# Kernel tuning notes

Hardware: AMD Instinct MI355X
Metric: run time of the kernel (lower is better)

The kernel has to match this reference:

```python
import jax, jax.numpy as jnp
import numpy as np

NQ, NKV, D = 32, 8, 64
HID = 2048
EPS = 1e-5
THETA = 1000000.0


def _rmsnorm(x, w):
    var = jnp.mean(x * x, axis=-1, keepdims=True)
    return x * jax.lax.rsqrt(var + EPS) * w


def setup_inputs() -> dict:
    key = jax.random.key(0)
    k1, k2, k3 = jax.random.split(key, 3)
    T = 2048
    positions = jnp.arange(T, dtype=jnp.int64) if jax.config.jax_enable_x64 else jnp.arange(T, dtype=jnp.int32)
    hidden_states = jax.random.normal(k1, (T, HID), dtype=jnp.float32)
    w_qkv = jax.random.normal(k2, (HID, (NQ + 2 * NKV) * D), dtype=jnp.float32) / np.sqrt(HID)
    w_out = jax.random.normal(k3, (NQ * D, HID), dtype=jnp.float32) / np.sqrt(NQ * D)
    q_ln_w = jnp.ones((D,), dtype=jnp.float32)
    k_ln_w = jnp.ones((D,), dtype=jnp.float32)
    return {"positions": positions, "hidden_states": hidden_states, "w_qkv": w_qkv,
            "w_out": w_out, "q_ln_w": q_ln_w, "k_ln_w": k_ln_w}


def reference(positions, hidden_states, w_qkv, w_out, q_ln_w, k_ln_w):
    T = hidden_states.shape[0]
    qkv = hidden_states @ w_qkv  # [T, (NQ+2*NKV)*D]
    q = qkv[:, : NQ * D].reshape(T, NQ, D)
    k = qkv[:, NQ * D : (NQ + NKV) * D].reshape(T, NKV, D)
    v = qkv[:, (NQ + NKV) * D :].reshape(T, NKV, D)
    # per-head RMSNorm on q and k
    q = _rmsnorm(q, q_ln_w)
    k = _rmsnorm(k, k_ln_w)
    # neox-style RoPE (rotate halves)
    inv_freq = 1.0 / (THETA ** (jnp.arange(0, D, 2, dtype=jnp.float32) / D))
    ang = positions.astype(jnp.float32)[:, None] * inv_freq  # [T, D/2]
    cos = jnp.cos(ang)[:, None, :]
    sin = jnp.sin(ang)[:, None, :]
    def rope(x):
        x1, x2 = x[..., : D // 2], x[..., D // 2 :]
        return jnp.concatenate([x1 * cos - x2 * sin, x2 * cos + x1 * sin], axis=-1)
    q = rope(q)
    k = rope(k)
    # grouped-query causal attention (one sequence, positions define order)
    G = NQ // NKV
    qg = q.reshape(T, NKV, G, D)
    scores = jnp.einsum('tkgd,skd->kgts', qg, k) * (D ** -0.5)  # [NKV,G,T,T]
    causal = jnp.arange(T)[:, None] >= jnp.arange(T)[None, :]
    scores = jnp.where(causal[None, None], scores, -1e30)
    probs = jax.nn.softmax(scores, axis=-1)
    attn = jnp.einsum('kgts,skd->tkgd', probs, v).reshape(T, NQ * D)
    return attn @ w_out
```

## Files before the change

### kernel.cpp

```cpp
#include <hip/hip_runtime.h>

typedef __bf16 bhalf;
typedef __bf16 bhalf8 __attribute__((ext_vector_type(8)));
typedef __bf16 bhalf4 __attribute__((ext_vector_type(4)));
typedef float f32x4 __attribute__((ext_vector_type(4)));

typedef __attribute__((address_space(1))) const void* gas_p;
typedef __attribute__((address_space(3))) void* las_p;

#define T_SEQ 2048
#define HIDN  2048
#define NQH   32
#define NKVH  8
#define DH    64
#define NQKV  3072

__global__ __launch_bounds__(256) void cast_bf16_k(const float* __restrict__ in,
                                                   bhalf* __restrict__ out, int n) {
  int i = (blockIdx.x * 256 + threadIdx.x) * 4;
  if (i + 3 < n) {
    float4 v = *(const float4*)(in + i);
    bhalf4 o;
    o[0] = (bhalf)v.x; o[1] = (bhalf)v.y; o[2] = (bhalf)v.z; o[3] = (bhalf)v.w;
    *(bhalf4*)(out + i) = o;
  }
}

__global__ __launch_bounds__(256) void transpose_cast_k(const float* __restrict__ in,
                                                        bhalf* __restrict__ out, int R, int C) {
  __shared__ float tile[32][33];
  int bx = blockIdx.x * 32;
  int by = blockIdx.y * 32;
  int tx = threadIdx.x & 31, ty = threadIdx.x >> 5;
#pragma unroll
  for (int p = 0; p < 4; ++p)
    tile[ty + 8 * p][tx] = in[(size_t)(by + ty + 8 * p) * C + bx + tx];
  __syncthreads();
#pragma unroll
  for (int p = 0; p < 4; ++p)
    out[(size_t)(bx + ty + 8 * p) * R + by + tx] = (bhalf)tile[tx][ty + 8 * p];
}

__global__ __launch_bounds__(256) void transpose_bf16_k(const bhalf* __restrict__ in,
                                                        bhalf* __restrict__ out, int R, int C) {
  __shared__ bhalf tile[32][33];
  int bx = blockIdx.x * 32;
  int by = blockIdx.y * 32;
  int tx = threadIdx.x & 31, ty = threadIdx.x >> 5;
#pragma unroll
  for (int p = 0; p < 4; ++p)
    tile[ty + 8 * p][tx] = in[(size_t)(by + ty + 8 * p) * C + bx + tx];
  __syncthreads();
#pragma unroll
  for (int p = 0; p < 4; ++p)
    out[(size_t)(bx + ty + 8 * p) * R + by + tx] = tile[tx][ty + 8 * p];
}

__device__ __forceinline__ void gemm_core(const bhalf* __restrict__ A,
                                          const bhalf* __restrict__ Bt, int K,
                                          int bm, int bn, int tid,
                                          bhalf* As, bhalf* Bs, f32x4 acc[2][4]) {
  int lane = tid & 63, wv = tid >> 6;
  int m16 = lane & 15, q4 = lane >> 4;
  int srow = tid >> 3;
  int scol = ((tid & 7) ^ (srow & 7)) * 8;
  const bhalf* asrc = A + (size_t)(bm + srow) * K + scol;
  const bhalf* bsrc = Bt + (size_t)(bn + srow) * K + scol;
  bhalf* adst = As + (wv * 8) * 64;
  bhalf* bdst = Bs + (wv * 8) * 64;
  int swz = m16 & 7;

  auto stage = [&](int k0, int sbuf) {
#pragma unroll
    for (int c = 0; c < 4; ++c)
      __builtin_amdgcn_global_load_lds((gas_p)(asrc + (size_t)(c * 32) * K + k0),
                                       (las_p)(adst + sbuf * 8192 + c * 2048), 16, 0, 0);
#pragma unroll
    for (int c = 0; c < 2; ++c)
      __builtin_amdgcn_global_load_lds((gas_p)(bsrc + (size_t)(c * 32) * K + k0),
                                       (las_p)(bdst + sbuf * 4096 + c * 2048), 16, 0, 0);
  };

  stage(0, 0);
  int buf = 0;
  for (int k0 = 0; k0 < K; k0 += 64) {
    __syncthreads();
    if (k0 + 64 < K) stage(k0 + 64, buf ^ 1);
    const bhalf* Ab = As + buf * 8192;
    const bhalf* Bb = Bs + buf * 4096;
    bhalf8 af[2][2], bf[4][2];
#pragma unroll
    for (int mi = 0; mi < 2; ++mi)
#pragma unroll
      for (int ks = 0; ks < 2; ++ks)
        af[mi][ks] = *(const bhalf8*)&Ab[(wv * 32 + mi * 16 + m16) * 64 +
                                         (((ks * 4 + q4) ^ swz) * 8)];
#pragma unroll
    for (int ni = 0; ni < 4; ++ni)
#pragma unroll
      for (int ks = 0; ks < 2; ++ks)
        bf[ni][ks] = *(const bhalf8*)&Bb[(ni * 16 + m16) * 64 +
                                         (((ks * 4 + q4) ^ swz) * 8)];
#pragma unroll
    for (int mi = 0; mi < 2; ++mi)
#pragma unroll
      for (int ni = 0; ni < 4; ++ni) {
        acc[mi][ni] = __builtin_amdgcn_mfma_f32_16x16x32_bf16(af[mi][0], bf[ni][0], acc[mi][ni], 0, 0, 0);
        acc[mi][ni] = __builtin_amdgcn_mfma_f32_16x16x32_bf16(af[mi][1], bf[ni][1], acc[mi][ni], 0, 0, 0);
      }
    buf ^= 1;
  }
}

__global__ __launch_bounds__(256) void gemm1_fused_k(const bhalf* __restrict__ A,
                                                     const bhalf* __restrict__ Bt,
                                                     const int* __restrict__ pos,
                                                     const float* __restrict__ qw,
                                                     const float* __restrict__ kw,
                                                     bhalf* __restrict__ qo,
                                                     bhalf* __restrict__ ko,
                                                     bhalf* __restrict__ vo) {
  __shared__ __align__(16) bhalf As[2 * 128 * 64];
  __shared__ __align__(16) bhalf Bs[2 * 64 * 64];
  int tid = threadIdx.x, lane = tid & 63, wv = tid >> 6;
  int m16 = lane & 15, q4 = lane >> 4;
  int bm = blockIdx.y * 128, bn = blockIdx.x * 64, h = blockIdx.x;
  f32x4 zero4 = {0.f, 0.f, 0.f, 0.f};
  f32x4 acc[2][4];
#pragma unroll
  for (int mi = 0; mi < 2; ++mi)
#pragma unroll
    for (int ni = 0; ni < 4; ++ni) acc[mi][ni] = zero4;

  gemm_core(A, Bt, HIDN, bm, bn, tid, As, Bs, acc);

  int wr0 = wv * 32;
  if (h < 40) {
    float wd[4];
    const float* wptr = (h < 32) ? qw : kw;
#pragma unroll
    for (int ni = 0; ni < 4; ++ni) wd[ni] = wptr[ni * 16 + m16];
    float f0 = exp2f((float)m16 * -0.6228615177913804f);
    float f1 = f0 * 0.001f;
#pragma unroll
    for (int mi = 0; mi < 2; ++mi)
#pragma unroll
      for (int r = 0; r < 4; ++r) {
        int trow = bm + wr0 + mi * 16 + q4 * 4 + r;
        float x0 = acc[mi][0][r], x1 = acc[mi][1][r], x2 = acc[mi][2][r], x3 = acc[mi][3][r];
        float ss = x0 * x0 + x1 * x1 + x2 * x2 + x3 * x3;
        ss += __shfl_xor(ss, 1);
        ss += __shfl_xor(ss, 2);
        ss += __shfl_xor(ss, 4);
        ss += __shfl_xor(ss, 8);
        float sc = rsqrtf(ss * (1.0f / 64.0f) + 1e-5f);
        float y0 = x0 * sc * wd[0], y1 = x1 * sc * wd[1];
        float y2 = x2 * sc * wd[2], y3 = x3 * sc * wd[3];
        float p = (float)pos[trow];
        float a0 = p * f0, a1 = p * f1;
        float c0 = cosf(a0), s0 = sinf(a0), c1 = cosf(a1), s1 = sinf(a1);
        float o0 = y0 * c0 - y2 * s0, o2 = y2 * c0 + y0 * s0;
        float o1 = y1 * c1 - y3 * s1, o3 = y3 * c1 + y1 * s1;
        bhalf* dst = (h < 32) ? (qo + (size_t)trow * 2048 + h * 64 + m16)
                              : (ko + (size_t)trow * 512 + (h - 32) * 64 + m16);
        dst[0] = (bhalf)o0; dst[16] = (bhalf)o1; dst[32] = (bhalf)o2; dst[48] = (bhalf)o3;
      }
  } else {
#pragma unroll
    for (int mi = 0; mi < 2; ++mi)
#pragma unroll
      for (int r = 0; r < 4; ++r) {
        int trow = bm + wr0 + mi * 16 + q4 * 4 + r;
        bhalf* dst = vo + (size_t)trow * 512 + (h - 40) * 64 + m16;
        dst[0] = (bhalf)acc[mi][0][r]; dst[16] = (bhalf)acc[mi][1][r];
        dst[32] = (bhalf)acc[mi][2][r]; dst[48] = (bhalf)acc[mi][3][r];
      }
  }
}

__global__ __launch_bounds__(256) void gemm2_k(const bhalf* __restrict__ A,
                                               const bhalf* __restrict__ Bt,
                                               float* __restrict__ C) {
  __shared__ __align__(16) bhalf As[2 * 128 * 64];
  __shared__ __align__(16) bhalf Bs[2 * 64 * 64];
  int tid = threadIdx.x, lane = tid & 63, wv = tid >> 6;
  int m16 = lane & 15, q4 = lane >> 4;
  int bm = blockIdx.y * 128, bn = blockIdx.x * 64;
  f32x4 zero4 = {0.f, 0.f, 0.f, 0.f};
  f32x4 acc[2][4];
#pragma unroll
  for (int mi = 0; mi < 2; ++mi)
#pragma unroll
    for (int ni = 0; ni < 4; ++ni) acc[mi][ni] = zero4;

  gemm_core(A, Bt, HIDN, bm, bn, tid, As, Bs, acc);

  int wr0 = wv * 32;
#pragma unroll
  for (int mi = 0; mi < 2; ++mi)
#pragma unroll
    for (int r = 0; r < 4; ++r) {
      size_t base = (size_t)(bm + wr0 + mi * 16 + q4 * 4 + r) * 2048 + bn + m16;
      C[base] = acc[mi][0][r]; C[base + 16] = acc[mi][1][r];
      C[base + 32] = acc[mi][2][r]; C[base + 48] = acc[mi][3][r];
    }
}

__global__ __launch_bounds__(256) void attn_k(const bhalf* __restrict__ q,
                                              const bhalf* __restrict__ k,
                                              const bhalf* __restrict__ vt,
                                              bhalf* __restrict__ o) {
  __shared__ __align__(16) bhalf Kb[2][4096];
  __shared__ __align__(16) bhalf Vb[2][4096];
  __shared__ __align__(16) bhalf Pb[4][16][72];
  int tid = threadIdx.x, lane = tid & 63, w = tid >> 6;
  int h = blockIdx.x, kh = h >> 2;
  int qt = 31 - blockIdx.y;
  int qb = qt * 64;
  int m16 = lane & 15, q4 = lane >> 4;
  int wrow0 = qb + w * 16;

  const float C1 = 0.18033688011112042f;
  const float C2 = 11.541560327111707f;

  const bhalf* qp = q + (size_t)(wrow0 + m16) * 2048 + h * 64;
  bhalf8 qf0 = *(const bhalf8*)(qp + q4 * 8);
  bhalf8 qf1 = *(const bhalf8*)(qp + 32 + q4 * 8);

  int srow = tid >> 3;
  int scol = ((tid & 7) ^ (srow & 7)) * 8;
  const bhalf* ksrc = k + (size_t)srow * 512 + kh * 64 + scol;
  const bhalf* vsrc = vt + (size_t)(kh * 64 + srow) * 2048 + scol;
  bhalf* kdst = &Kb[0][0] + w * 512;
  bhalf* vdst = &Vb[0][0] + w * 512;

  auto stage = [&](int c) {
    int buf = c & 1, s0 = c * 64;
#pragma unroll
    for (int j = 0; j < 2; ++j) {
      __builtin_amdgcn_global_load_lds((gas_p)(ksrc + (size_t)(s0 + j * 32) * 512),
                                       (las_p)(kdst + buf * 4096 + j * 2048), 16, 0, 0);
      __builtin_amdgcn_global_load_lds((gas_p)(vsrc + (size_t)(j * 32) * 2048 + s0),
                                       (las_p)(vdst + buf * 4096 + j * 2048), 16, 0, 0);
    }
  };

  f32x4 zero4 = {0.f, 0.f, 0.f, 0.f};
  f32x4 oac[4];
  float psum = 0.f;
#pragma unroll
  for (int ni = 0; ni < 4; ++ni) oac[ni] = zero4;
  int swz = m16 & 7;
  bhalf* pwr = &Pb[w][m16][q4 * 4];
  const bhalf* par = &Pb[w][m16][q4 * 8];

  stage(0);
  for (int c = 0; c <= qt; ++c) {
    __syncthreads();
    if (c < qt) stage(c + 1);
    int buf = c & 1, s0 = c * 64;
    if (c < qt) {
      bhalf8 kf[4][2];
#pragma unroll
      for (int st = 0; st < 4; ++st)
#pragma unroll
        for (int ks = 0; ks < 2; ++ks)
          kf[st][ks] = *(const bhalf8*)&Kb[buf][(st * 16 + m16) * 64 + (((ks * 4 + q4) ^ swz) * 8)];
      f32x4 sv[4];
      __builtin_amdgcn_s_setprio(1);
#pragma unroll
      for (int st = 0; st < 4; ++st) {
        f32x4 t0 = __builtin_amdgcn_mfma_f32_16x16x32_bf16(kf[st][0], qf0, zero4, 0, 0, 0);
        sv[st] = __builtin_amdgcn_mfma_f32_16x16x32_bf16(kf[st][1], qf1, t0, 0, 0, 0);
      }
      __builtin_amdgcn_s_setprio(0);
#pragma unroll
      for (int st = 0; st < 4; ++st) {
        bhalf4 pk;
#pragma unroll
        for (int r = 0; r < 4; ++r) {
          float pe = exp2f(sv[st][r] * C1 - C2);
          psum += pe;
          pk[r] = (bhalf)pe;
        }
        *(bhalf4*)(pwr + st * 16) = pk;
      }
      bhalf8 vf[4][2];
#pragma unroll
      for (int ni = 0; ni < 4; ++ni)
#pragma unroll
        for (int ks = 0; ks < 2; ++ks)
          vf[ni][ks] = *(const bhalf8*)&Vb[buf][(ni * 16 + m16) * 64 + (((ks * 4 + q4) ^ swz) * 8)];
      bhalf8 ap0 = *(const bhalf8*)par;
      bhalf8 ap1 = *(const bhalf8*)(par + 32);
      __builtin_amdgcn_s_setprio(1);
#pragma unroll
      for (int ni = 0; ni < 4; ++ni) {
        oac[ni] = __builtin_amdgcn_mfma_f32_16x16x32_bf16(ap0, vf[ni][0], oac[ni], 0, 0, 0);
        oac[ni] = __builtin_amdgcn_mfma_f32_16x16x32_bf16(ap1, vf[ni][1], oac[ni], 0, 0, 0);
      }
      __builtin_amdgcn_s_setprio(0);
    } else {
      bhalf8 kf[4][2];
      f32x4 sv[4];
#pragma unroll
      for (int st = 0; st < 4; ++st)
        if (st <= w) {
#pragma unroll
          for (int ks = 0; ks < 2; ++ks)
            kf[st][ks] = *(const bhalf8*)&Kb[buf][(st * 16 + m16) * 64 + (((ks * 4 + q4) ^ swz) * 8)];
          f32x4 t0 = __builtin_amdgcn_mfma_f32_16x16x32_bf16(kf[st][0], qf0, zero4, 0, 0, 0);
          sv[st] = __builtin_amdgcn_mfma_f32_16x16x32_bf16(kf[st][1], qf1, t0, 0, 0, 0);
        }
      int stwr = (w >= 2) ? 3 : 1;
#pragma unroll
      for (int st = 0; st < 4; ++st) {
        if (st > stwr) continue;
        bhalf4 pk;
#pragma unroll
        for (int r = 0; r < 4; ++r) {
          float pe = 0.f;
          if (st < w) {
            pe = exp2f(sv[st][r] * C1 - C2);
          } else if (st == w) {
            pe = (q4 * 4 + r <= m16) ? exp2f(sv[st][r] * C1 - C2) : 0.f;
          }
          psum += pe;
          pk[r] = (bhalf)pe;
        }
        *(bhalf4*)(pwr + st * 16) = pk;
      }
      int ksmax = (w >= 2) ? 1 : 0;
      bhalf8 vf[4][2];
#pragma unroll
      for (int ni = 0; ni < 4; ++ni)
#pragma unroll
        for (int ks = 0; ks < 2; ++ks)
          if (ks <= ksmax)
            vf[ni][ks] = *(const bhalf8*)&Vb[buf][(ni * 16 + m16) * 64 + (((ks * 4 + q4) ^ swz) * 8)];
      bhalf8 ap0 = *(const bhalf8*)par;
#pragma unroll
      for (int ni = 0; ni < 4; ++ni)
        oac[ni] = __builtin_amdgcn_mfma_f32_16x16x32_bf16(ap0, vf[ni][0], oac[ni], 0, 0, 0);
      if (ksmax) {
        bhalf8 ap1 = *(const bhalf8*)(par + 32);
#pragma unroll
        for (int ni = 0; ni < 4; ++ni)
          oac[ni] = __builtin_amdgcn_mfma_f32_16x16x32_bf16(ap1, vf[ni][1], oac[ni], 0, 0, 0);
      }
    }
  }
  psum += __shfl_xor(psum, 16);
  psum += __shfl_xor(psum, 32);
  float inv = 1.0f / psum;
  float invr[4];
#pragma unroll
  for (int r = 0; r < 4; ++r) invr[r] = __shfl(inv, q4 * 4 + r);
#pragma unroll
  for (int ni = 0; ni < 4; ++ni)
#pragma unroll
    for (int r = 0; r < 4; ++r) {
      int trow = wrow0 + q4 * 4 + r;
      o[(size_t)trow * 2048 + h * 64 + ni * 16 + m16] = (bhalf)(oac[ni][r] * invr[r]);
    }
}

extern "C" void kernel_launch(void* const* d_in, const int* in_sizes, int n_in,
                              void* d_out, int out_size, void* d_ws, size_t ws_size,
                              hipStream_t stream) {
  const int* positions = (const int*)d_in[0];
  const float* hidden  = (const float*)d_in[1];
  const float* w_qkv   = (const float*)d_in[2];
  const float* w_out   = (const float*)d_in[3];
  const float* q_ln    = (const float*)d_in[4];
  const float* k_ln    = (const float*)d_in[5];
  float* out = (float*)d_out;

  char* wsp = (char*)d_ws;
  bhalf* hid_bf  = (bhalf*)(wsp);
  bhalf* wqkvT   = (bhalf*)(wsp + 8388608);
  bhalf* woutT   = (bhalf*)(wsp + 20971520);
  bhalf* q_bf    = (bhalf*)(wsp + 29360128);
  bhalf* k_bf    = (bhalf*)(wsp + 37748736);
  bhalf* v_bf    = (bhalf*)(wsp + 39845888);
  bhalf* vt_g    = (bhalf*)(wsp + 41943040);
  bhalf* attn_bf = (bhalf*)(wsp + 44040192);

  cast_bf16_k<<<T_SEQ * HIDN / 1024, 256, 0, stream>>>(hidden, hid_bf, T_SEQ * HIDN);
  transpose_cast_k<<<dim3(NQKV / 32, HIDN / 32), 256, 0, stream>>>(w_qkv, wqkvT, HIDN, NQKV);
  transpose_cast_k<<<dim3(HIDN / 32, HIDN / 32), 256, 0, stream>>>(w_out, woutT, HIDN, HIDN);
  gemm1_fused_k<<<dim3(NQKV / 64, T_SEQ / 128), 256, 0, stream>>>(
      hid_bf, wqkvT, positions, q_ln, k_ln, q_bf, k_bf, v_bf);
  transpose_bf16_k<<<dim3(512 / 32, T_SEQ / 32), 256, 0, stream>>>(v_bf, vt_g, T_SEQ, 512);
  attn_k<<<dim3(NQH, 32), 256, 0, stream>>>(q_bf, k_bf, vt_g, attn_bf);
  gemm2_k<<<dim3(HIDN / 64, T_SEQ / 128), 256, 0, stream>>>(attn_bf, woutT, out);
}
```

Before: 222.0 us.

## Write V transposed from QKV GEMM epilogue, fold softmax scale into q norm

The QKV GEMM epilogue now writes V directly in the transposed [d, t] layout with packed 4-element stores. This removes the separate bf16 transpose kernel and its extra global round trip. The softmax scale is folded into the q RMSNorm weight and the constant max-offset subtraction is dropped, saving an FMA per score in the attention loop. The P staging buffer switches from row padding to an XOR swizzle, which shrinks LDS use. The risks are larger exp2 arguments, which stay bounded because q and k are normalized, and strided 8-byte V stores in the epilogue.

After: 217.4 us. -2.1%, faster.

```diff
diff --git a/kernel.cpp b/kernel.cpp
--- a/kernel.cpp
+++ b/kernel.cpp
@@ -39,21 +39,6 @@
 #pragma unroll
   for (int p = 0; p < 4; ++p)
     out[(size_t)(bx + ty + 8 * p) * R + by + tx] = (bhalf)tile[tx][ty + 8 * p];
-}
-
-__global__ __launch_bounds__(256) void transpose_bf16_k(const bhalf* __restrict__ in,
-                                                        bhalf* __restrict__ out, int R, int C) {
-  __shared__ bhalf tile[32][33];
-  int bx = blockIdx.x * 32;
-  int by = blockIdx.y * 32;
-  int tx = threadIdx.x & 31, ty = threadIdx.x >> 5;
-#pragma unroll
-  for (int p = 0; p < 4; ++p)
-    tile[ty + 8 * p][tx] = in[(size_t)(by + ty + 8 * p) * C + bx + tx];
-  __syncthreads();
-#pragma unroll
-  for (int p = 0; p < 4; ++p)
-    out[(size_t)(bx + ty + 8 * p) * R + by + tx] = tile[tx][ty + 8 * p];
 }
 
 __device__ __forceinline__ void gemm_core(const bhalf* __restrict__ A,
@@ -119,7 +104,7 @@
                                                      const float* __restrict__ kw,
                                                      bhalf* __restrict__ qo,
                                                      bhalf* __restrict__ ko,
-                                                     bhalf* __restrict__ vo) {
+                                                     bhalf* __restrict__ vt) {
   __shared__ __align__(16) bhalf As[2 * 128 * 64];
   __shared__ __align__(16) bhalf Bs[2 * 64 * 64];
   int tid = threadIdx.x, lane = tid & 63, wv = tid >> 6;
@@ -138,8 +123,9 @@
   if (h < 40) {
     float wd[4];
     const float* wptr = (h < 32) ? qw : kw;
-#pragma unroll
-    for (int ni = 0; ni < 4; ++ni) wd[ni] = wptr[ni * 16 + m16];
+    float wscale = (h < 32) ? 0.18033688011112042f : 1.0f;
+#pragma unroll
+    for (int ni = 0; ni < 4; ++ni) wd[ni] = wptr[ni * 16 + m16] * wscale;
     float f0 = exp2f((float)m16 * -0.6228615177913804f);
     float f1 = f0 * 0.001f;
 #pragma unroll
@@ -169,11 +155,13 @@
 #pragma unroll
     for (int mi = 0; mi < 2; ++mi)
 #pragma unroll
-      for (int r = 0; r < 4; ++r) {
-        int trow = bm + wr0 + mi * 16 + q4 * 4 + r;
-        bhalf* dst = vo + (size_t)trow * 512 + (h - 40) * 64 + m16;
-        dst[0] = (bhalf)acc[mi][0][r]; dst[16] = (bhalf)acc[mi][1][r];
-        dst[32] = (bhalf)acc[mi][2][r]; dst[48] = (bhalf)acc[mi][3][r];
+      for (int ni = 0; ni < 4; ++ni) {
+        int trow0 = bm + wr0 + mi * 16 + q4 * 4;
+        int d = (h - 40) * 64 + ni * 16 + m16;
+        bhalf4 pk;
+        pk[0] = (bhalf)acc[mi][ni][0]; pk[1] = (bhalf)acc[mi][ni][1];
+        pk[2] = (bhalf)acc[mi][ni][2]; pk[3] = (bhalf)acc[mi][ni][3];
+        *(bhalf4*)(vt + (size_t)d * 2048 + trow0) = pk;
       }
   }
 }
@@ -212,16 +200,13 @@
                                               bhalf* __restrict__ o) {
   __shared__ __align__(16) bhalf Kb[2][4096];
   __shared__ __align__(16) bhalf Vb[2][4096];
-  __shared__ __align__(16) bhalf Pb[4][16][72];
+  __shared__ __align__(16) bhalf Pb[4][16][64];
   int tid = threadIdx.x, lane = tid & 63, w = tid >> 6;
   int h = blockIdx.x, kh = h >> 2;
   int qt = 31 - blockIdx.y;
   int qb = qt * 64;
   int m16 = lane & 15, q4 = lane >> 4;
   int wrow0 = qb + w * 16;
-
-  const float C1 = 0.18033688011112042f;
-  const float C2 = 11.541560327111707f;
 
   const bhalf* qp = q + (size_t)(wrow0 + m16) * 2048 + h * 64;
   bhalf8 qf0 = *(const bhalf8*)(qp + q4 * 8);
@@ -251,14 +236,14 @@
 #pragma unroll
   for (int ni = 0; ni < 4; ++ni) oac[ni] = zero4;
   int swz = m16 & 7;
-  bhalf* pwr = &Pb[w][m16][q4 * 4];
-  const bhalf* par = &Pb[w][m16][q4 * 8];
+  bhalf* prow = &Pb[w][m16][0];
+  int woff = (q4 & 1) << 2;
 
   stage(0);
   for (int c = 0; c <= qt; ++c) {
     __syncthreads();
     if (c < qt) stage(c + 1);
-    int buf = c & 1, s0 = c * 64;
+    int buf = c & 1;
     if (c < qt) {
       bhalf8 kf[4][2];
 #pragma unroll
@@ -279,11 +264,11 @@
         bhalf4 pk;
 #pragma unroll
         for (int r = 0; r < 4; ++r) {
-          float pe = exp2f(sv[st][r] * C1 - C2);
+          float pe = exp2f(sv[st][r]);
           psum += pe;
           pk[r] = (bhalf)pe;
         }
-        *(bhalf4*)(pwr + st * 16) = pk;
+        *(bhalf4*)(prow + ((((2 * st + (q4 >> 1)) ^ swz) << 3) + woff)) = pk;
       }
       bhalf8 vf[4][2];
 #pragma unroll
@@ -291,8 +276,8 @@
 #pragma unroll
         for (int ks = 0; ks < 2; ++ks)
           vf[ni][ks] = *(const bhalf8*)&Vb[buf][(ni * 16 + m16) * 64 + (((ks * 4 + q4) ^ swz) * 8)];
-      bhalf8 ap0 = *(const bhalf8*)par;
-      bhalf8 ap1 = *(const bhalf8*)(par + 32);
+      bhalf8 ap0 = *(const bhalf8*)(prow + ((q4 ^ swz) << 3));
+      bhalf8 ap1 = *(const bhalf8*)(prow + (((4 + q4) ^ swz) << 3));
       __builtin_amdgcn_s_setprio(1);
 #pragma unroll
       for (int ni = 0; ni < 4; ++ni) {
@@ -321,14 +306,14 @@
         for (int r = 0; r < 4; ++r) {
           float pe = 0.f;
           if (st < w) {
-            pe = exp2f(sv[st][r] * C1 - C2);
+            pe = exp2f(sv[st][r]);
           } else if (st == w) {
-            pe = (q4 * 4 + r <= m16) ? exp2f(sv[st][r] * C1 - C2) : 0.f;
+            pe = (q4 * 4 + r <= m16) ? exp2f(sv[st][r]) : 0.f;
           }
           psum += pe;
           pk[r] = (bhalf)pe;
         }
-        *(bhalf4*)(pwr + st * 16) = pk;
+        *(bhalf4*)(prow + ((((2 * st + (q4 >> 1)) ^ swz) << 3) + woff)) = pk;
       }
       int ksmax = (w >= 2) ? 1 : 0;
       bhalf8 vf[4][2];
@@ -338,12 +323,12 @@
         for (int ks = 0; ks < 2; ++ks)
           if (ks <= ksmax)
             vf[ni][ks] = *(const bhalf8*)&Vb[buf][(ni * 16 + m16) * 64 + (((ks * 4 + q4) ^ swz) * 8)];
-      bhalf8 ap0 = *(const bhalf8*)par;
+      bhalf8 ap0 = *(const bhalf8*)(prow + ((q4 ^ swz) << 3));
 #pragma unroll
       for (int ni = 0; ni < 4; ++ni)
         oac[ni] = __builtin_amdgcn_mfma_f32_16x16x32_bf16(ap0, vf[ni][0], oac[ni], 0, 0, 0);
       if (ksmax) {
-        bhalf8 ap1 = *(const bhalf8*)(par + 32);
+        bhalf8 ap1 = *(const bhalf8*)(prow + (((4 + q4) ^ swz) << 3));
 #pragma unroll
         for (int ni = 0; ni < 4; ++ni)
           oac[ni] = __builtin_amdgcn_mfma_f32_16x16x32_bf16(ap1, vf[ni][1], oac[ni], 0, 0, 0);
@@ -382,7 +367,6 @@
   bhalf* woutT   = (bhalf*)(wsp + 20971520);
   bhalf* q_bf    = (bhalf*)(wsp + 29360128);
   bhalf* k_bf    = (bhalf*)(wsp + 37748736);
-  bhalf* v_bf    = (bhalf*)(wsp + 39845888);
   bhalf* vt_g    = (bhalf*)(wsp + 41943040);
   bhalf* attn_bf = (bhalf*)(wsp + 44040192);
 
@@ -390,8 +374,7 @@
   transpose_cast_k<<<dim3(NQKV / 32, HIDN / 32), 256, 0, stream>>>(w_qkv, wqkvT, HIDN, NQKV);
   transpose_cast_k<<<dim3(HIDN / 32, HIDN / 32), 256, 0, stream>>>(w_out, woutT, HIDN, HIDN);
   gemm1_fused_k<<<dim3(NQKV / 64, T_SEQ / 128), 256, 0, stream>>>(
-      hid_bf, wqkvT, positions, q_ln, k_ln, q_bf, k_bf, v_bf);
-  transpose_bf16_k<<<dim3(512 / 32, T_SEQ / 32), 256, 0, stream>>>(v_bf, vt_g, T_SEQ, 512);
+      hid_bf, wqkvT, positions, q_ln, k_ln, q_bf, k_bf, vt_g);
   attn_k<<<dim3(NQH, 32), 256, 0, stream>>>(q_bf, k_bf, vt_g, attn_bf);
   gemm2_k<<<dim3(HIDN / 64, T_SEQ / 128), 256, 0, stream>>>(attn_bf, woutT, out);
 }
```
